# Kernel optimization log

Measured on AMD Instinct MI355X. Metric: run time of the kernel, lower is better.

## Reference

```python
import jax, jax.numpy as jnp
import numpy as np

N_NODES = 100000
N_EDGES = 3200000
EMB_DIM = 128


def setup_inputs() -> dict:
    key = jax.random.key(0)
    k_emb, k_w1, k_w2, k_e = jax.random.split(key, 4)
    emb = jax.random.normal(k_emb, (N_NODES, EMB_DIM), dtype=jnp.float32)
    W1 = jax.random.normal(k_w1, (EMB_DIM, 64), dtype=jnp.float32) * (1.0 / np.sqrt(EMB_DIM))
    b1 = jnp.zeros((64,), dtype=jnp.float32)
    W2 = jax.random.normal(k_w2, (64, 32), dtype=jnp.float32) * (1.0 / np.sqrt(64))
    b2 = jnp.zeros((32,), dtype=jnp.float32)
    edge_index = jax.random.randint(k_e, (2, N_EDGES), 0, N_NODES, dtype=jnp.int64)
    return {"embedding": emb, "W1": W1, "b1": b1, "W2": W2, "b2": b2,
            "edge_index": edge_index}


def gcn_conv(x, W, b, src, dst, n):
    # PyG GCNConv defaults: add self-loops, symmetric normalization D^-1/2 (A+I) D^-1/2,
    # linear transform first, then gather-scale-scatter aggregation, then bias.
    xw = x @ W                                                  # [N, out]
    ones = jnp.ones(src.shape, dtype=xw.dtype)
    deg = jax.ops.segment_sum(ones, dst, num_segments=n) + 1.0  # in-degree + self-loop
    dis = jax.lax.rsqrt(deg)                                    # deg >= 1 always
    norm = dis[src] * dis[dst]                                  # [E]
    agg = jax.ops.segment_sum(xw[src] * norm[:, None], dst, num_segments=n)
    agg = agg + (dis * dis)[:, None] * xw                       # self-loop messages
    return agg + b


def reference(embedding, W1, b1, W2, b2, edge_index):
    n = embedding.shape[0]
    src, dst = edge_index[0], edge_index[1]
    # encode
    h = jax.nn.relu(gcn_conv(embedding, W1, b1, src, dst, n))
    z = gcn_conv(h, W2, b2, src, dst, n)                        # [N, 32]
    # decode: per-edge gather-dot-sigmoid
    logits = jnp.sum(z[src] * z[dst], axis=1)                   # [E]
    return jax.nn.sigmoid(logits)
```

## Files before the change

kernel.cpp:

```cpp
#include <hip/hip_runtime.h>
#include <hip/hip_bf16.h>
#include <math.h>

#define NN 100000
#define NE 3200000
#define NPAD 100096
#define NB 196
#define BN 512
#define EPB 8192
#define NBLK 391

typedef __attribute__((ext_vector_type(8))) short short8;
typedef __attribute__((ext_vector_type(4))) float floatx4;

__device__ __forceinline__ unsigned short bf16_of(float x) {
    __hip_bfloat16 h = __float2bfloat16(x);
    return *(unsigned short*)&h;
}
__device__ __forceinline__ unsigned pack2(float a, float b) {
    return (unsigned)bf16_of(a) | ((unsigned)bf16_of(b) << 16);
}
__device__ __forceinline__ float lo_f(unsigned u) { return __uint_as_float(u << 16); }
__device__ __forceinline__ float hi_f(unsigned u) { return __uint_as_float(u & 0xffff0000u); }
__device__ __forceinline__ void acc8(float* a, uint4 r) {
    a[0] += lo_f(r.x); a[1] += hi_f(r.x);
    a[2] += lo_f(r.y); a[3] += hi_f(r.y);
    a[4] += lo_f(r.z); a[5] += hi_f(r.z);
    a[6] += lo_f(r.w); a[7] += hi_f(r.w);
}

__global__ __launch_bounds__(256) void hist_kernel(const int* __restrict__ dst,
                                                   int* __restrict__ blkhist) {
    __shared__ int cnt[NB];
    int t = threadIdx.x;
    for (int i = t; i < NB; i += 256) cnt[i] = 0;
    __syncthreads();
    int e0 = blockIdx.x * EPB;
    int e1 = min(e0 + EPB, NE);
    for (int e = e0 + t; e < e1; e += 256) atomicAdd(&cnt[dst[e] >> 9], 1);
    __syncthreads();
    for (int i = t; i < NB; i += 256) blkhist[i * NBLK + blockIdx.x] = cnt[i];
}

__global__ __launch_bounds__(64) void scanA_kernel(int* __restrict__ blkhist,
                                                   int* __restrict__ totals) {
    int j = blockIdx.x, lane = threadIdx.x;
    int base = j * NBLK;
    int carry = 0;
    for (int c = 0; c < NBLK; c += 64) {
        int b = c + lane;
        int v = (b < NBLK) ? blkhist[base + b] : 0;
        int inc = v;
#pragma unroll
        for (int m = 1; m < 64; m <<= 1) {
            int u = __shfl_up(inc, m, 64);
            if (lane >= m) inc += u;
        }
        if (b < NBLK) blkhist[base + b] = carry + inc - v;
        carry += __shfl(inc, 63, 64);
    }
    if (lane == 0) totals[j] = carry;
}

__global__ __launch_bounds__(256) void scanB_kernel(const int* __restrict__ totals,
                                                    int* __restrict__ bucket_base) {
    __shared__ int sm[NB];
    int t = threadIdx.x;
    if (t < NB) sm[t] = totals[t];
    __syncthreads();
    if (t == 0) {
        int r = 0;
        for (int i = 0; i < NB; ++i) { bucket_base[i] = r; r += sm[i]; }
        bucket_base[NB] = r;
    }
}

__global__ __launch_bounds__(256) void scatter_kernel(const int* __restrict__ src,
                                                      const int* __restrict__ dst,
                                                      const int* __restrict__ blkhist,
                                                      const int* __restrict__ bucket_base,
                                                      int* __restrict__ staged) {
    __shared__ int cnt[NB];
    __shared__ int lbase[NB + 1];
    __shared__ int gbase[NB];
    __shared__ int sbuf[EPB];
    __shared__ unsigned char sbkt[EPB];
    int t = threadIdx.x;
    for (int i = t; i < NB; i += 256) cnt[i] = 0;
    __syncthreads();
    int e0 = blockIdx.x * EPB;
    int e1 = min(e0 + EPB, NE);
    int cn = e1 - e0;
    for (int e = e0 + t; e < e1; e += 256) atomicAdd(&cnt[dst[e] >> 9], 1);
    __syncthreads();
    if (t < 64) {
        int v[4]; int s = 0;
#pragma unroll
        for (int k = 0; k < 4; ++k) { int idx = t * 4 + k; v[k] = (idx < NB) ? cnt[idx] : 0; s += v[k]; }
        int inc = s;
#pragma unroll
        for (int m = 1; m < 64; m <<= 1) {
            int u = __shfl_up(inc, m, 64);
            if (t >= m) inc += u;
        }
        int run = inc - s;
#pragma unroll
        for (int k = 0; k < 4; ++k) { int idx = t * 4 + k; if (idx < NB) lbase[idx] = run; run += v[k]; }
        if (t == 63) lbase[NB] = inc;
    }
    __syncthreads();
    for (int i = t; i < NB; i += 256) {
        gbase[i] = bucket_base[i] + blkhist[i * NBLK + blockIdx.x];
        cnt[i] = lbase[i];
    }
    __syncthreads();
    for (int e = e0 + t; e < e1; e += 256) {
        int s = src[e], d = dst[e];
        int bk = d >> 9;
        int r = atomicAdd(&cnt[bk], 1);
        sbuf[r] = (s << 9) | (d & (BN - 1));
        sbkt[r] = (unsigned char)bk;
    }
    __syncthreads();
    for (int i = t; i < cn; i += 256) {
        int bk = sbkt[i];
        staged[gbase[bk] + i - lbase[bk]] = sbuf[i];
    }
}

__global__ __launch_bounds__(256) void fine_kernel(const int* __restrict__ staged,
                                                   const int* __restrict__ bucket_base,
                                                   int* __restrict__ offset,
                                                   float* __restrict__ dis,
                                                   int* __restrict__ csr_src) {
    __shared__ int hist[BN];
    __shared__ int offs[BN];
    __shared__ int cur[BN];
    int t = threadIdx.x, j = blockIdx.x;
    int bb = bucket_base[j], be = bucket_base[j + 1];
    for (int i = t; i < BN; i += 256) hist[i] = 0;
    __syncthreads();
    for (int e = bb + t; e < be; e += 256) atomicAdd(&hist[staged[e] & (BN - 1)], 1);
    __syncthreads();
    if (t < 64) {
        int v[8]; int s = 0;
#pragma unroll
        for (int k = 0; k < 8; ++k) { v[k] = hist[t * 8 + k]; s += v[k]; }
        int inc = s;
#pragma unroll
        for (int m = 1; m < 64; m <<= 1) {
            int u = __shfl_up(inc, m, 64);
            if (t >= m) inc += u;
        }
        int run = inc - s;
#pragma unroll
        for (int k = 0; k < 8; ++k) { offs[t * 8 + k] = run; run += v[k]; }
    }
    __syncthreads();
    for (int l = t; l < BN; l += 256) {
        cur[l] = offs[l];
        int n = j * BN + l;
        if (n < NN) {
            offset[n] = bb + offs[l];
            dis[n] = rsqrtf((float)hist[l] + 1.0f);
        }
    }
    if (j == NB - 1 && t == 0) offset[NN] = NE;
    __syncthreads();
    for (int e = bb + t; e < be; e += 256) {
        int p = staged[e];
        int r = atomicAdd(&cur[p & (BN - 1)], 1);
        csr_src[bb + r] = p >> 9;
    }
}

__global__ __launch_bounds__(256) void mm1_kernel(const float* __restrict__ x,
                                                  const float* __restrict__ W,
                                                  const float* __restrict__ dis,
                                                  unsigned short* __restrict__ y) {
    __shared__ unsigned short Wt[64][136];
    int t = threadIdx.x;
    for (int i = t; i < 128 * 64; i += 256) {
        int k = i >> 6, n = i & 63;
        Wt[n][k] = bf16_of(W[i]);
    }
    __syncthreads();
    int wave = t >> 6, lane = t & 63;
    int quad = lane >> 4, n16 = lane & 15;
    short8 bfr[4][4];
#pragma unroll
    for (int s = 0; s < 4; ++s)
#pragma unroll
        for (int tt = 0; tt < 4; ++tt)
            bfr[s][tt] = *(const short8*)&Wt[tt * 16 + n16][s * 32 + quad * 8];
    int tile0 = (blockIdx.x * 4 + wave) * 4;
#pragma unroll 1
    for (int it = 0; it < 4; ++it) {
        int tile = tile0 + it;
        if (tile >= 6250) break;
        int m0 = tile * 16;
        const float* xp = x + (size_t)(m0 + n16) * 128 + quad * 8;
        floatx4 acc0 = {0,0,0,0}, acc1 = {0,0,0,0}, acc2 = {0,0,0,0}, acc3 = {0,0,0,0};
#pragma unroll
        for (int s = 0; s < 4; ++s) {
            float4 lo = *(const float4*)(xp + s * 32);
            float4 hi = *(const float4*)(xp + s * 32 + 4);
            short8 a;
            a[0] = (short)bf16_of(lo.x); a[1] = (short)bf16_of(lo.y);
            a[2] = (short)bf16_of(lo.z); a[3] = (short)bf16_of(lo.w);
            a[4] = (short)bf16_of(hi.x); a[5] = (short)bf16_of(hi.y);
            a[6] = (short)bf16_of(hi.z); a[7] = (short)bf16_of(hi.w);
            acc0 = __builtin_amdgcn_mfma_f32_16x16x32_bf16(a, bfr[s][0], acc0, 0, 0, 0);
            acc1 = __builtin_amdgcn_mfma_f32_16x16x32_bf16(a, bfr[s][1], acc1, 0, 0, 0);
            acc2 = __builtin_amdgcn_mfma_f32_16x16x32_bf16(a, bfr[s][2], acc2, 0, 0, 0);
            acc3 = __builtin_amdgcn_mfma_f32_16x16x32_bf16(a, bfr[s][3], acc3, 0, 0, 0);
        }
#pragma unroll
        for (int r = 0; r < 4; ++r) {
            int ro = m0 + quad * 4 + r;
            float sc = dis[ro];
            unsigned short* yp = y + (size_t)ro * 64 + n16;
            yp[0]  = bf16_of(acc0[r] * sc);
            yp[16] = bf16_of(acc1[r] * sc);
            yp[32] = bf16_of(acc2[r] * sc);
            yp[48] = bf16_of(acc3[r] * sc);
        }
    }
}

__global__ __launch_bounds__(256) void mm2_kernel(const unsigned short* __restrict__ h,
                                                  const float* __restrict__ W,
                                                  const float* __restrict__ dis,
                                                  unsigned short* __restrict__ y) {
    __shared__ unsigned short Wt[32][72];
    int t = threadIdx.x;
    for (int i = t; i < 64 * 32; i += 256) {
        int k = i >> 5, n = i & 31;
        Wt[n][k] = bf16_of(W[i]);
    }
    __syncthreads();
    int wave = t >> 6, lane = t & 63;
    int quad = lane >> 4, n16 = lane & 15;
    short8 bfr[2][2];
#pragma unroll
    for (int s = 0; s < 2; ++s)
#pragma unroll
        for (int tt = 0; tt < 2; ++tt)
            bfr[s][tt] = *(const short8*)&Wt[tt * 16 + n16][s * 32 + quad * 8];
    int tile0 = (blockIdx.x * 4 + wave) * 4;
#pragma unroll 1
    for (int it = 0; it < 4; ++it) {
        int tile = tile0 + it;
        if (tile >= 6250) break;
        int m0 = tile * 16;
        const unsigned short* hp = h + (size_t)(m0 + n16) * 64 + quad * 8;
        floatx4 acc0 = {0,0,0,0}, acc1 = {0,0,0,0};
#pragma unroll
        for (int s = 0; s < 2; ++s) {
            short8 a = *(const short8*)(hp + s * 32);
            acc0 = __builtin_amdgcn_mfma_f32_16x16x32_bf16(a, bfr[s][0], acc0, 0, 0, 0);
            acc1 = __builtin_amdgcn_mfma_f32_16x16x32_bf16(a, bfr[s][1], acc1, 0, 0, 0);
        }
#pragma unroll
        for (int r = 0; r < 4; ++r) {
            int ro = m0 + quad * 4 + r;
            float sc = dis[ro];
            unsigned short* yp = y + (size_t)ro * 32 + n16;
            yp[0]  = bf16_of(acc0[r] * sc);
            yp[16] = bf16_of(acc1[r] * sc);
        }
    }
}

__global__ __launch_bounds__(256) void agg64_kernel(const uint4* __restrict__ ys4,
                                                    const float* __restrict__ dis,
                                                    const int* __restrict__ offset,
                                                    const int* __restrict__ csr_src,
                                                    const float* __restrict__ b,
                                                    uint4* __restrict__ h4) {
    int tid = blockIdx.x * 256 + threadIdx.x;
    int nd = tid >> 3, c = tid & 7;
    if (nd >= NN) return;
    int start = offset[nd], end = offset[nd + 1];
    float acc[8] = {0, 0, 0, 0, 0, 0, 0, 0};
    acc8(acc, ys4[(size_t)nd * 8 + c]);
    int i = start;
    int n8 = start + ((end - start) & ~7);
    for (; i < n8; i += 8) {
        int s0 = csr_src[i],     s1 = csr_src[i + 1], s2 = csr_src[i + 2], s3 = csr_src[i + 3];
        int s4 = csr_src[i + 4], s5 = csr_src[i + 5], s6 = csr_src[i + 6], s7 = csr_src[i + 7];
        uint4 r0 = ys4[(size_t)s0 * 8 + c];
        uint4 r1 = ys4[(size_t)s1 * 8 + c];
        uint4 r2 = ys4[(size_t)s2 * 8 + c];
        uint4 r3 = ys4[(size_t)s3 * 8 + c];
        uint4 r4 = ys4[(size_t)s4 * 8 + c];
        uint4 r5 = ys4[(size_t)s5 * 8 + c];
        uint4 r6 = ys4[(size_t)s6 * 8 + c];
        uint4 r7 = ys4[(size_t)s7 * 8 + c];
        acc8(acc, r0); acc8(acc, r1); acc8(acc, r2); acc8(acc, r3);
        acc8(acc, r4); acc8(acc, r5); acc8(acc, r6); acc8(acc, r7);
    }
    for (; i < end; ++i) acc8(acc, ys4[(size_t)csr_src[i] * 8 + c]);
    float ds = dis[nd];
    const float4 bv0 = *(const float4*)&b[c * 8];
    const float4 bv1 = *(const float4*)&b[c * 8 + 4];
    uint4 o;
    o.x = pack2(fmaxf(fmaf(ds, acc[0], bv0.x), 0.f), fmaxf(fmaf(ds, acc[1], bv0.y), 0.f));
    o.y = pack2(fmaxf(fmaf(ds, acc[2], bv0.z), 0.f), fmaxf(fmaf(ds, acc[3], bv0.w), 0.f));
    o.z = pack2(fmaxf(fmaf(ds, acc[4], bv1.x), 0.f), fmaxf(fmaf(ds, acc[5], bv1.y), 0.f));
    o.w = pack2(fmaxf(fmaf(ds, acc[6], bv1.z), 0.f), fmaxf(fmaf(ds, acc[7], bv1.w), 0.f));
    h4[(size_t)nd * 8 + c] = o;
}

__global__ __launch_bounds__(256) void agg32_kernel(const uint4* __restrict__ ys4,
                                                    const float* __restrict__ dis,
                                                    const int* __restrict__ offset,
                                                    const int* __restrict__ csr_src,
                                                    const float* __restrict__ b,
                                                    uint4* __restrict__ z4) {
    int tid = blockIdx.x * 256 + threadIdx.x;
    int nd = tid >> 2, c = tid & 3;
    if (nd >= NN) return;
    int start = offset[nd], end = offset[nd + 1];
    float acc[8] = {0, 0, 0, 0, 0, 0, 0, 0};
    acc8(acc, ys4[(size_t)nd * 4 + c]);
    int i = start;
    int n8 = start + ((end - start) & ~7);
    for (; i < n8; i += 8) {
        int s0 = csr_src[i],     s1 = csr_src[i + 1], s2 = csr_src[i + 2], s3 = csr_src[i + 3];
        int s4 = csr_src[i + 4], s5 = csr_src[i + 5], s6 = csr_src[i + 6], s7 = csr_src[i + 7];
        uint4 r0 = ys4[(size_t)s0 * 4 + c];
        uint4 r1 = ys4[(size_t)s1 * 4 + c];
        uint4 r2 = ys4[(size_t)s2 * 4 + c];
        uint4 r3 = ys4[(size_t)s3 * 4 + c];
        uint4 r4 = ys4[(size_t)s4 * 4 + c];
        uint4 r5 = ys4[(size_t)s5 * 4 + c];
        uint4 r6 = ys4[(size_t)s6 * 4 + c];
        uint4 r7 = ys4[(size_t)s7 * 4 + c];
        acc8(acc, r0); acc8(acc, r1); acc8(acc, r2); acc8(acc, r3);
        acc8(acc, r4); acc8(acc, r5); acc8(acc, r6); acc8(acc, r7);
    }
    for (; i < end; ++i) acc8(acc, ys4[(size_t)csr_src[i] * 4 + c]);
    float ds = dis[nd];
    const float4 bv0 = *(const float4*)&b[c * 8];
    const float4 bv1 = *(const float4*)&b[c * 8 + 4];
    uint4 o;
    o.x = pack2(fmaf(ds, acc[0], bv0.x), fmaf(ds, acc[1], bv0.y));
    o.y = pack2(fmaf(ds, acc[2], bv0.z), fmaf(ds, acc[3], bv0.w));
    o.z = pack2(fmaf(ds, acc[4], bv1.x), fmaf(ds, acc[5], bv1.y));
    o.w = pack2(fmaf(ds, acc[6], bv1.z), fmaf(ds, acc[7], bv1.w));
    z4[(size_t)nd * 4 + c] = o;
}

__global__ __launch_bounds__(256) void decode_kernel(const uint4* __restrict__ z4,
                                                     const int* __restrict__ src,
                                                     const int* __restrict__ dst,
                                                     float* __restrict__ out) {
    int tid = blockIdx.x * 256 + threadIdx.x;
    int e = tid >> 2, k = tid & 3;
    if (e >= NE) return;
    int s = src[e], d = dst[e];
    uint4 ra = z4[(size_t)s * 4 + k];
    uint4 rb = z4[(size_t)d * 4 + k];
    float acc;
    acc  = lo_f(ra.x) * lo_f(rb.x) + hi_f(ra.x) * hi_f(rb.x);
    acc += lo_f(ra.y) * lo_f(rb.y) + hi_f(ra.y) * hi_f(rb.y);
    acc += lo_f(ra.z) * lo_f(rb.z) + hi_f(ra.z) * hi_f(rb.z);
    acc += lo_f(ra.w) * lo_f(rb.w) + hi_f(ra.w) * hi_f(rb.w);
#pragma unroll
    for (int m = 2; m >= 1; m >>= 1) acc += __shfl_xor(acc, m, 4);
    if (k == 0) out[e] = 1.0f / (1.0f + expf(-acc));
}

extern "C" void kernel_launch(void* const* d_in, const int* in_sizes, int n_in,
                              void* d_out, int out_size, void* d_ws, size_t ws_size,
                              hipStream_t stream) {
    const float* emb = (const float*)d_in[0];
    const float* W1  = (const float*)d_in[1];
    const float* b1  = (const float*)d_in[2];
    const float* W2  = (const float*)d_in[3];
    const float* b2  = (const float*)d_in[4];
    const int*   ei  = (const int*)d_in[5];
    const int* src = ei;
    const int* dst = ei + NE;
    float* out = (float*)d_out;

    char* w = (char*)d_ws;
    int*   offset      = (int*)w;           w += (size_t)NPAD * 4;
    float* dis         = (float*)w;         w += (size_t)NPAD * 4;
    int*   bucket_base = (int*)w;           w += 1024;
    int*   totals      = (int*)w;           w += 1024;
    int*   blkhist     = (int*)w;           w += 307200;
    int*   csr_src     = (int*)w;           w += (size_t)NE * 4;
    int*   staged      = (int*)w;           w += (size_t)NE * 4;
    unsigned short* ysbuf = (unsigned short*)w; w += (size_t)NN * 64 * 2;
    unsigned short* h  = (unsigned short*)w;
    unsigned short* ys1 = ysbuf;
    unsigned short* ys2 = ysbuf;
    unsigned short* z   = ysbuf + (size_t)NN * 32;

    hist_kernel<<<NBLK, 256, 0, stream>>>(dst, blkhist);
    scanA_kernel<<<NB, 64, 0, stream>>>(blkhist, totals);
    scanB_kernel<<<1, 256, 0, stream>>>(totals, bucket_base);
    scatter_kernel<<<NBLK, 256, 0, stream>>>(src, dst, blkhist, bucket_base, staged);
    fine_kernel<<<NB, 256, 0, stream>>>(staged, bucket_base, offset, dis, csr_src);

    mm1_kernel<<<391, 256, 0, stream>>>(emb, W1, dis, ys1);
    agg64_kernel<<<(NN * 8) / 256, 256, 0, stream>>>((const uint4*)ys1, dis, offset, csr_src, b1, (uint4*)h);

    mm2_kernel<<<391, 256, 0, stream>>>(h, W2, dis, ys2);
    agg32_kernel<<<(NN * 4 + 255) / 256, 256, 0, stream>>>((const uint4*)ys2, dis, offset, csr_src, b2, (uint4*)z);

    decode_kernel<<<(NE * 4) / 256, 256, 0, stream>>>((const uint4*)z, src, dst, out);
}
```

Measured before the change: 363.3 us.

## Split feature tables into 16-column chunks for cache-resident gathers; finer CSR buckets

Stores the transformed node features in a column-chunked layout (16 bf16 columns per chunk, one 3.2 MB slab per chunk) so each aggregation and decode pass gathers from a table small enough to stay in cache. Aggregation becomes one generic kernel launched per chunk, and decode runs in two passes that accumulate a partial dot product in a scratch buffer. The CSR build also moves to 256-node buckets and stages each bucket in LDS in the fine kernel to avoid re-reading it from global memory. The cost is more kernel launches, rereading the CSR indices and edge lists once per chunk, and an extra partial-sum round trip in decode.

```diff
diff --git a/kernel.cpp b/kernel.cpp
--- a/kernel.cpp
+++ b/kernel.cpp
@@ -5,10 +5,11 @@
 #define NN 100000
 #define NE 3200000
 #define NPAD 100096
-#define NB 196
-#define BN 512
+#define NB 391
+#define BN 256
 #define EPB 8192
 #define NBLK 391
+#define SBUF 9728
 
 typedef __attribute__((ext_vector_type(8))) short short8;
 typedef __attribute__((ext_vector_type(4))) float floatx4;
@@ -22,12 +23,6 @@
 }
 __device__ __forceinline__ float lo_f(unsigned u) { return __uint_as_float(u << 16); }
 __device__ __forceinline__ float hi_f(unsigned u) { return __uint_as_float(u & 0xffff0000u); }
-__device__ __forceinline__ void acc8(float* a, uint4 r) {
-    a[0] += lo_f(r.x); a[1] += hi_f(r.x);
-    a[2] += lo_f(r.y); a[3] += hi_f(r.y);
-    a[4] += lo_f(r.z); a[5] += hi_f(r.z);
-    a[6] += lo_f(r.w); a[7] += hi_f(r.w);
-}
 
 __global__ __launch_bounds__(256) void hist_kernel(const int* __restrict__ dst,
                                                    int* __restrict__ blkhist) {
@@ -37,7 +32,7 @@
     __syncthreads();
     int e0 = blockIdx.x * EPB;
     int e1 = min(e0 + EPB, NE);
-    for (int e = e0 + t; e < e1; e += 256) atomicAdd(&cnt[dst[e] >> 9], 1);
+    for (int e = e0 + t; e < e1; e += 256) atomicAdd(&cnt[dst[e] >> 8], 1);
     __syncthreads();
     for (int i = t; i < NB; i += 256) blkhist[i * NBLK + blockIdx.x] = cnt[i];
 }
@@ -66,7 +61,7 @@
                                                     int* __restrict__ bucket_base) {
     __shared__ int sm[NB];
     int t = threadIdx.x;
-    if (t < NB) sm[t] = totals[t];
+    for (int i = t; i < NB; i += 256) sm[i] = totals[i];
     __syncthreads();
     if (t == 0) {
         int r = 0;
@@ -84,19 +79,19 @@
     __shared__ int lbase[NB + 1];
     __shared__ int gbase[NB];
     __shared__ int sbuf[EPB];
-    __shared__ unsigned char sbkt[EPB];
+    __shared__ unsigned short sbkt[EPB];
     int t = threadIdx.x;
     for (int i = t; i < NB; i += 256) cnt[i] = 0;
     __syncthreads();
     int e0 = blockIdx.x * EPB;
     int e1 = min(e0 + EPB, NE);
     int cn = e1 - e0;
-    for (int e = e0 + t; e < e1; e += 256) atomicAdd(&cnt[dst[e] >> 9], 1);
+    for (int e = e0 + t; e < e1; e += 256) atomicAdd(&cnt[dst[e] >> 8], 1);
     __syncthreads();
     if (t < 64) {
-        int v[4]; int s = 0;
-#pragma unroll
-        for (int k = 0; k < 4; ++k) { int idx = t * 4 + k; v[k] = (idx < NB) ? cnt[idx] : 0; s += v[k]; }
+        int v[7]; int s = 0;
+#pragma unroll
+        for (int k = 0; k < 7; ++k) { int idx = t * 7 + k; v[k] = (idx < NB) ? cnt[idx] : 0; s += v[k]; }
         int inc = s;
 #pragma unroll
         for (int m = 1; m < 64; m <<= 1) {
@@ -105,7 +100,7 @@
         }
         int run = inc - s;
 #pragma unroll
-        for (int k = 0; k < 4; ++k) { int idx = t * 4 + k; if (idx < NB) lbase[idx] = run; run += v[k]; }
+        for (int k = 0; k < 7; ++k) { int idx = t * 7 + k; if (idx < NB) lbase[idx] = run; run += v[k]; }
         if (t == 63) lbase[NB] = inc;
     }
     __syncthreads();
@@ -116,10 +111,10 @@
     __syncthreads();
     for (int e = e0 + t; e < e1; e += 256) {
         int s = src[e], d = dst[e];
-        int bk = d >> 9;
+        int bk = d >> 8;
         int r = atomicAdd(&cnt[bk], 1);
-        sbuf[r] = (s << 9) | (d & (BN - 1));
-        sbkt[r] = (unsigned char)bk;
+        sbuf[r] = (s << 8) | (d & (BN - 1));
+        sbkt[r] = (unsigned short)bk;
     }
     __syncthreads();
     for (int i = t; i < cn; i += 256) {
@@ -136,16 +131,27 @@
     __shared__ int hist[BN];
     __shared__ int offs[BN];
     __shared__ int cur[BN];
+    __shared__ int sb[SBUF];
     int t = threadIdx.x, j = blockIdx.x;
     int bb = bucket_base[j], be = bucket_base[j + 1];
+    int cn = be - bb;
+    bool lds_ok = (cn <= SBUF);
     for (int i = t; i < BN; i += 256) hist[i] = 0;
     __syncthreads();
-    for (int e = bb + t; e < be; e += 256) atomicAdd(&hist[staged[e] & (BN - 1)], 1);
+    if (lds_ok) {
+        for (int e = t; e < cn; e += 256) {
+            int p = staged[bb + e];
+            sb[e] = p;
+            atomicAdd(&hist[p & (BN - 1)], 1);
+        }
+    } else {
+        for (int e = t; e < cn; e += 256) atomicAdd(&hist[staged[bb + e] & (BN - 1)], 1);
+    }
     __syncthreads();
     if (t < 64) {
-        int v[8]; int s = 0;
-#pragma unroll
-        for (int k = 0; k < 8; ++k) { v[k] = hist[t * 8 + k]; s += v[k]; }
+        int v[4]; int s = 0;
+#pragma unroll
+        for (int k = 0; k < 4; ++k) { v[k] = hist[t * 4 + k]; s += v[k]; }
         int inc = s;
 #pragma unroll
         for (int m = 1; m < 64; m <<= 1) {
@@ -154,23 +160,23 @@
         }
         int run = inc - s;
 #pragma unroll
-        for (int k = 0; k < 8; ++k) { offs[t * 8 + k] = run; run += v[k]; }
-    }
-    __syncthreads();
-    for (int l = t; l < BN; l += 256) {
-        cur[l] = offs[l];
-        int n = j * BN + l;
+        for (int k = 0; k < 4; ++k) { offs[t * 4 + k] = run; run += v[k]; }
+    }
+    __syncthreads();
+    if (t < BN) {
+        cur[t] = offs[t];
+        int n = j * BN + t;
         if (n < NN) {
-            offset[n] = bb + offs[l];
-            dis[n] = rsqrtf((float)hist[l] + 1.0f);
+            offset[n] = bb + offs[t];
+            dis[n] = rsqrtf((float)hist[t] + 1.0f);
         }
     }
     if (j == NB - 1 && t == 0) offset[NN] = NE;
     __syncthreads();
-    for (int e = bb + t; e < be; e += 256) {
-        int p = staged[e];
+    for (int e = t; e < cn; e += 256) {
+        int p = lds_ok ? sb[e] : staged[bb + e];
         int r = atomicAdd(&cur[p & (BN - 1)], 1);
-        csr_src[bb + r] = p >> 9;
+        csr_src[bb + r] = p >> 8;
     }
 }
 
@@ -219,11 +225,10 @@
         for (int r = 0; r < 4; ++r) {
             int ro = m0 + quad * 4 + r;
             float sc = dis[ro];
-            unsigned short* yp = y + (size_t)ro * 64 + n16;
-            yp[0]  = bf16_of(acc0[r] * sc);
-            yp[16] = bf16_of(acc1[r] * sc);
-            yp[32] = bf16_of(acc2[r] * sc);
-            yp[48] = bf16_of(acc3[r] * sc);
+            y[((size_t)0 * NN + ro) * 16 + n16] = bf16_of(acc0[r] * sc);
+            y[((size_t)1 * NN + ro) * 16 + n16] = bf16_of(acc1[r] * sc);
+            y[((size_t)2 * NN + ro) * 16 + n16] = bf16_of(acc2[r] * sc);
+            y[((size_t)3 * NN + ro) * 16 + n16] = bf16_of(acc3[r] * sc);
         }
     }
 }
@@ -253,11 +258,12 @@
         int tile = tile0 + it;
         if (tile >= 6250) break;
         int m0 = tile * 16;
-        const unsigned short* hp = h + (size_t)(m0 + n16) * 64 + quad * 8;
         floatx4 acc0 = {0,0,0,0}, acc1 = {0,0,0,0};
 #pragma unroll
         for (int s = 0; s < 2; ++s) {
-            short8 a = *(const short8*)(hp + s * 32);
+            const unsigned short* hp =
+                h + ((size_t)(s * 2 + (quad >> 1)) * NN + (m0 + n16)) * 16 + (quad & 1) * 8;
+            short8 a = *(const short8*)hp;
             acc0 = __builtin_amdgcn_mfma_f32_16x16x32_bf16(a, bfr[s][0], acc0, 0, 0, 0);
             acc1 = __builtin_amdgcn_mfma_f32_16x16x32_bf16(a, bfr[s][1], acc1, 0, 0, 0);
         }
@@ -265,111 +271,70 @@
         for (int r = 0; r < 4; ++r) {
             int ro = m0 + quad * 4 + r;
             float sc = dis[ro];
-            unsigned short* yp = y + (size_t)ro * 32 + n16;
-            yp[0]  = bf16_of(acc0[r] * sc);
-            yp[16] = bf16_of(acc1[r] * sc);
-        }
-    }
-}
-
-__global__ __launch_bounds__(256) void agg64_kernel(const uint4* __restrict__ ys4,
-                                                    const float* __restrict__ dis,
-                                                    const int* __restrict__ offset,
-                                                    const int* __restrict__ csr_src,
-                                                    const float* __restrict__ b,
-                                                    uint4* __restrict__ h4) {
+            y[((size_t)0 * NN + ro) * 16 + n16] = bf16_of(acc0[r] * sc);
+            y[((size_t)1 * NN + ro) * 16 + n16] = bf16_of(acc1[r] * sc);
+        }
+    }
+}
+
+__global__ __launch_bounds__(256) void aggc_kernel(const unsigned* __restrict__ ysp,
+                                                   const float* __restrict__ dis,
+                                                   const int* __restrict__ offset,
+                                                   const int* __restrict__ csr_src,
+                                                   const float* __restrict__ b,
+                                                   unsigned* __restrict__ outp,
+                                                   int do_relu) {
     int tid = blockIdx.x * 256 + threadIdx.x;
-    int nd = tid >> 3, c = tid & 7;
+    int nd = tid >> 3, c8 = tid & 7;
     if (nd >= NN) return;
     int start = offset[nd], end = offset[nd + 1];
-    float acc[8] = {0, 0, 0, 0, 0, 0, 0, 0};
-    acc8(acc, ys4[(size_t)nd * 8 + c]);
+    float a0, a1;
+    { unsigned u = ysp[nd * 8 + c8]; a0 = lo_f(u); a1 = hi_f(u); }
     int i = start;
     int n8 = start + ((end - start) & ~7);
     for (; i < n8; i += 8) {
         int s0 = csr_src[i],     s1 = csr_src[i + 1], s2 = csr_src[i + 2], s3 = csr_src[i + 3];
         int s4 = csr_src[i + 4], s5 = csr_src[i + 5], s6 = csr_src[i + 6], s7 = csr_src[i + 7];
-        uint4 r0 = ys4[(size_t)s0 * 8 + c];
-        uint4 r1 = ys4[(size_t)s1 * 8 + c];
-        uint4 r2 = ys4[(size_t)s2 * 8 + c];
-        uint4 r3 = ys4[(size_t)s3 * 8 + c];
-        uint4 r4 = ys4[(size_t)s4 * 8 + c];
-        uint4 r5 = ys4[(size_t)s5 * 8 + c];
-        uint4 r6 = ys4[(size_t)s6 * 8 + c];
-        uint4 r7 = ys4[(size_t)s7 * 8 + c];
-        acc8(acc, r0); acc8(acc, r1); acc8(acc, r2); acc8(acc, r3);
-        acc8(acc, r4); acc8(acc, r5); acc8(acc, r6); acc8(acc, r7);
-    }
-    for (; i < end; ++i) acc8(acc, ys4[(size_t)csr_src[i] * 8 + c]);
+        unsigned u0 = ysp[s0 * 8 + c8], u1 = ysp[s1 * 8 + c8];
+        unsigned u2 = ysp[s2 * 8 + c8], u3 = ysp[s3 * 8 + c8];
+        unsigned u4 = ysp[s4 * 8 + c8], u5 = ysp[s5 * 8 + c8];
+        unsigned u6 = ysp[s6 * 8 + c8], u7 = ysp[s7 * 8 + c8];
+        a0 += lo_f(u0); a1 += hi_f(u0); a0 += lo_f(u1); a1 += hi_f(u1);
+        a0 += lo_f(u2); a1 += hi_f(u2); a0 += lo_f(u3); a1 += hi_f(u3);
+        a0 += lo_f(u4); a1 += hi_f(u4); a0 += lo_f(u5); a1 += hi_f(u5);
+        a0 += lo_f(u6); a1 += hi_f(u6); a0 += lo_f(u7); a1 += hi_f(u7);
+    }
+    for (; i < end; ++i) {
+        unsigned u = ysp[csr_src[i] * 8 + c8];
+        a0 += lo_f(u); a1 += hi_f(u);
+    }
     float ds = dis[nd];
-    const float4 bv0 = *(const float4*)&b[c * 8];
-    const float4 bv1 = *(const float4*)&b[c * 8 + 4];
-    uint4 o;
-    o.x = pack2(fmaxf(fmaf(ds, acc[0], bv0.x), 0.f), fmaxf(fmaf(ds, acc[1], bv0.y), 0.f));
-    o.y = pack2(fmaxf(fmaf(ds, acc[2], bv0.z), 0.f), fmaxf(fmaf(ds, acc[3], bv0.w), 0.f));
-    o.z = pack2(fmaxf(fmaf(ds, acc[4], bv1.x), 0.f), fmaxf(fmaf(ds, acc[5], bv1.y), 0.f));
-    o.w = pack2(fmaxf(fmaf(ds, acc[6], bv1.z), 0.f), fmaxf(fmaf(ds, acc[7], bv1.w), 0.f));
-    h4[(size_t)nd * 8 + c] = o;
-}
-
-__global__ __launch_bounds__(256) void agg32_kernel(const uint4* __restrict__ ys4,
-                                                    const float* __restrict__ dis,
-                                                    const int* __restrict__ offset,
-                                                    const int* __restrict__ csr_src,
-                                                    const float* __restrict__ b,
-                                                    uint4* __restrict__ z4) {
-    int tid = blockIdx.x * 256 + threadIdx.x;
-    int nd = tid >> 2, c = tid & 3;
-    if (nd >= NN) return;
-    int start = offset[nd], end = offset[nd + 1];
-    float acc[8] = {0, 0, 0, 0, 0, 0, 0, 0};
-    acc8(acc, ys4[(size_t)nd * 4 + c]);
-    int i = start;
-    int n8 = start + ((end - start) & ~7);
-    for (; i < n8; i += 8) {
-        int s0 = csr_src[i],     s1 = csr_src[i + 1], s2 = csr_src[i + 2], s3 = csr_src[i + 3];
-        int s4 = csr_src[i + 4], s5 = csr_src[i + 5], s6 = csr_src[i + 6], s7 = csr_src[i + 7];
-        uint4 r0 = ys4[(size_t)s0 * 4 + c];
-        uint4 r1 = ys4[(size_t)s1 * 4 + c];
-        uint4 r2 = ys4[(size_t)s2 * 4 + c];
-        uint4 r3 = ys4[(size_t)s3 * 4 + c];
-        uint4 r4 = ys4[(size_t)s4 * 4 + c];
-        uint4 r5 = ys4[(size_t)s5 * 4 + c];
-        uint4 r6 = ys4[(size_t)s6 * 4 + c];
-        uint4 r7 = ys4[(size_t)s7 * 4 + c];
-        acc8(acc, r0); acc8(acc, r1); acc8(acc, r2); acc8(acc, r3);
-        acc8(acc, r4); acc8(acc, r5); acc8(acc, r6); acc8(acc, r7);
-    }
-    for (; i < end; ++i) acc8(acc, ys4[(size_t)csr_src[i] * 4 + c]);
-    float ds = dis[nd];
-    const float4 bv0 = *(const float4*)&b[c * 8];
-    const float4 bv1 = *(const float4*)&b[c * 8 + 4];
-    uint4 o;
-    o.x = pack2(fmaf(ds, acc[0], bv0.x), fmaf(ds, acc[1], bv0.y));
-    o.y = pack2(fmaf(ds, acc[2], bv0.z), fmaf(ds, acc[3], bv0.w));
-    o.z = pack2(fmaf(ds, acc[4], bv1.x), fmaf(ds, acc[5], bv1.y));
-    o.w = pack2(fmaf(ds, acc[6], bv1.z), fmaf(ds, acc[7], bv1.w));
-    z4[(size_t)nd * 4 + c] = o;
-}
-
-__global__ __launch_bounds__(256) void decode_kernel(const uint4* __restrict__ z4,
-                                                     const int* __restrict__ src,
-                                                     const int* __restrict__ dst,
-                                                     float* __restrict__ out) {
+    float r0 = fmaf(ds, a0, b[c8 * 2]);
+    float r1 = fmaf(ds, a1, b[c8 * 2 + 1]);
+    if (do_relu) { r0 = fmaxf(r0, 0.f); r1 = fmaxf(r1, 0.f); }
+    outp[nd * 8 + c8] = pack2(r0, r1);
+}
+
+__global__ __launch_bounds__(256) void decodec_kernel(const uint2* __restrict__ zp,
+                                                      const int* __restrict__ src,
+                                                      const int* __restrict__ dst,
+                                                      float* __restrict__ partial,
+                                                      float* __restrict__ out,
+                                                      int final_) {
     int tid = blockIdx.x * 256 + threadIdx.x;
     int e = tid >> 2, k = tid & 3;
     if (e >= NE) return;
     int s = src[e], d = dst[e];
-    uint4 ra = z4[(size_t)s * 4 + k];
-    uint4 rb = z4[(size_t)d * 4 + k];
-    float acc;
-    acc  = lo_f(ra.x) * lo_f(rb.x) + hi_f(ra.x) * hi_f(rb.x);
-    acc += lo_f(ra.y) * lo_f(rb.y) + hi_f(ra.y) * hi_f(rb.y);
-    acc += lo_f(ra.z) * lo_f(rb.z) + hi_f(ra.z) * hi_f(rb.z);
-    acc += lo_f(ra.w) * lo_f(rb.w) + hi_f(ra.w) * hi_f(rb.w);
-#pragma unroll
-    for (int m = 2; m >= 1; m >>= 1) acc += __shfl_xor(acc, m, 4);
-    if (k == 0) out[e] = 1.0f / (1.0f + expf(-acc));
+    uint2 za = zp[s * 4 + k];
+    uint2 zb = zp[d * 4 + k];
+    float acc = lo_f(za.x) * lo_f(zb.x) + hi_f(za.x) * hi_f(zb.x)
+              + lo_f(za.y) * lo_f(zb.y) + hi_f(za.y) * hi_f(zb.y);
+    acc += __shfl_xor(acc, 1, 4);
+    acc += __shfl_xor(acc, 2, 4);
+    if (k == 0) {
+        if (!final_) partial[e] = acc;
+        else out[e] = 1.0f / (1.0f + expf(-(partial[e] + acc)));
+    }
 }
 
 extern "C" void kernel_launch(void* const* d_in, const int* in_sizes, int n_in,
@@ -388,9 +353,9 @@
     char* w = (char*)d_ws;
     int*   offset      = (int*)w;           w += (size_t)NPAD * 4;
     float* dis         = (float*)w;         w += (size_t)NPAD * 4;
-    int*   bucket_base = (int*)w;           w += 1024;
-    int*   totals      = (int*)w;           w += 1024;
-    int*   blkhist     = (int*)w;           w += 307200;
+    int*   bucket_base = (int*)w;           w += 2048;
+    int*   totals      = (int*)w;           w += 2048;
+    int*   blkhist     = (int*)w;           w += (size_t)NB * NBLK * 4 + 1024;
     int*   csr_src     = (int*)w;           w += (size_t)NE * 4;
     int*   staged      = (int*)w;           w += (size_t)NE * 4;
     unsigned short* ysbuf = (unsigned short*)w; w += (size_t)NN * 64 * 2;
@@ -398,6 +363,7 @@
     unsigned short* ys1 = ysbuf;
     unsigned short* ys2 = ysbuf;
     unsigned short* z   = ysbuf + (size_t)NN * 32;
+    float* partial = (float*)staged;
 
     hist_kernel<<<NBLK, 256, 0, stream>>>(dst, blkhist);
     scanA_kernel<<<NB, 64, 0, stream>>>(blkhist, totals);
@@ -406,10 +372,18 @@
     fine_kernel<<<NB, 256, 0, stream>>>(staged, bucket_base, offset, dis, csr_src);
 
     mm1_kernel<<<391, 256, 0, stream>>>(emb, W1, dis, ys1);
-    agg64_kernel<<<(NN * 8) / 256, 256, 0, stream>>>((const uint4*)ys1, dis, offset, csr_src, b1, (uint4*)h);
+    for (int c = 0; c < 4; ++c)
+        aggc_kernel<<<(NN * 8 + 255) / 256, 256, 0, stream>>>(
+            (const unsigned*)(ys1 + (size_t)c * NN * 16), dis, offset, csr_src,
+            b1 + c * 16, (unsigned*)(h + (size_t)c * NN * 16), 1);
 
     mm2_kernel<<<391, 256, 0, stream>>>(h, W2, dis, ys2);
-    agg32_kernel<<<(NN * 4 + 255) / 256, 256, 0, stream>>>((const uint4*)ys2, dis, offset, csr_src, b2, (uint4*)z);
-
-    decode_kernel<<<(NE * 4) / 256, 256, 0, stream>>>((const uint4*)z, src, dst, out);
-}
+    for (int c = 0; c < 2; ++c)
+        aggc_kernel<<<(NN * 8 + 255) / 256, 256, 0, stream>>>(
+            (const unsigned*)(ys2 + (size_t)c * NN * 16), dis, offset, csr_src,
+            b2 + c * 16, (unsigned*)(z + (size_t)c * NN * 16), 0);
+
+    for (int p = 0; p < 2; ++p)
+        decodec_kernel<<<(NE * 4) / 256, 256, 0, stream>>>(
+            (const uint2*)(z + (size_t)p * NN * 16), src, dst, partial, out, p);
+}
```

New measurement: 446.2 us. +22.8%, slower.

## Decode edges in CSR order per destination node with fp16 dot2

Applied to the files above, without the earlier changes.

The decode stage now walks the CSR built for aggregation. One wavefront per destination node loads that node's z row once and reuses it across all incoming edges, and results are written back through a stored original edge id. This removes the random gather of z[dst] per edge but adds scattered output stores plus an extra edge-id array that must be staged and written. z is now stored as fp16 instead of bf16 so the dot product can use the packed fdot2 instruction. The bucket sort is rebuilt with 256-node buckets and 4096-edge scatter blocks, and it carries 8-byte staged entries.

```diff
diff --git a/kernel.cpp b/kernel.cpp
--- a/kernel.cpp
+++ b/kernel.cpp
@@ -5,13 +5,14 @@
 #define NN 100000
 #define NE 3200000
 #define NPAD 100096
-#define NB 196
-#define BN 512
-#define EPB 8192
-#define NBLK 391
+#define NB 391
+#define BN 256
+#define EPB 4096
+#define SBLK 782
 
 typedef __attribute__((ext_vector_type(8))) short short8;
 typedef __attribute__((ext_vector_type(4))) float floatx4;
+typedef _Float16 h2_t __attribute__((ext_vector_type(2)));
 
 __device__ __forceinline__ unsigned short bf16_of(float x) {
     __hip_bfloat16 h = __float2bfloat16(x);
@@ -29,6 +30,21 @@
     a[6] += lo_f(r.w); a[7] += hi_f(r.w);
 }
 
+__device__ __forceinline__ unsigned packh2(float a, float b) {
+    unsigned short ua = __builtin_bit_cast(unsigned short, (_Float16)a);
+    unsigned short ub = __builtin_bit_cast(unsigned short, (_Float16)b);
+    return (unsigned)ua | ((unsigned)ub << 16);
+}
+__device__ __forceinline__ float dot2acc(unsigned a, unsigned b, float acc) {
+#if __has_builtin(__builtin_amdgcn_fdot2)
+    return __builtin_amdgcn_fdot2(__builtin_bit_cast(h2_t, a),
+                                  __builtin_bit_cast(h2_t, b), acc, false);
+#else
+    h2_t ha = __builtin_bit_cast(h2_t, a), hb = __builtin_bit_cast(h2_t, b);
+    return acc + (float)ha[0] * (float)hb[0] + (float)ha[1] * (float)hb[1];
+#endif
+}
+
 __global__ __launch_bounds__(256) void hist_kernel(const int* __restrict__ dst,
                                                    int* __restrict__ blkhist) {
     __shared__ int cnt[NB];
@@ -37,26 +53,26 @@
     __syncthreads();
     int e0 = blockIdx.x * EPB;
     int e1 = min(e0 + EPB, NE);
-    for (int e = e0 + t; e < e1; e += 256) atomicAdd(&cnt[dst[e] >> 9], 1);
-    __syncthreads();
-    for (int i = t; i < NB; i += 256) blkhist[i * NBLK + blockIdx.x] = cnt[i];
+    for (int e = e0 + t; e < e1; e += 256) atomicAdd(&cnt[dst[e] >> 8], 1);
+    __syncthreads();
+    for (int i = t; i < NB; i += 256) blkhist[i * SBLK + blockIdx.x] = cnt[i];
 }
 
 __global__ __launch_bounds__(64) void scanA_kernel(int* __restrict__ blkhist,
                                                    int* __restrict__ totals) {
     int j = blockIdx.x, lane = threadIdx.x;
-    int base = j * NBLK;
+    int base = j * SBLK;
     int carry = 0;
-    for (int c = 0; c < NBLK; c += 64) {
+    for (int c = 0; c < SBLK; c += 64) {
         int b = c + lane;
-        int v = (b < NBLK) ? blkhist[base + b] : 0;
+        int v = (b < SBLK) ? blkhist[base + b] : 0;
         int inc = v;
 #pragma unroll
         for (int m = 1; m < 64; m <<= 1) {
             int u = __shfl_up(inc, m, 64);
             if (lane >= m) inc += u;
         }
-        if (b < NBLK) blkhist[base + b] = carry + inc - v;
+        if (b < SBLK) blkhist[base + b] = carry + inc - v;
         carry += __shfl(inc, 63, 64);
     }
     if (lane == 0) totals[j] = carry;
@@ -66,7 +82,7 @@
                                                     int* __restrict__ bucket_base) {
     __shared__ int sm[NB];
     int t = threadIdx.x;
-    if (t < NB) sm[t] = totals[t];
+    for (int i = t; i < NB; i += 256) sm[i] = totals[i];
     __syncthreads();
     if (t == 0) {
         int r = 0;
@@ -79,24 +95,24 @@
                                                       const int* __restrict__ dst,
                                                       const int* __restrict__ blkhist,
                                                       const int* __restrict__ bucket_base,
-                                                      int* __restrict__ staged) {
+                                                      int2* __restrict__ staged) {
     __shared__ int cnt[NB];
     __shared__ int lbase[NB + 1];
     __shared__ int gbase[NB];
-    __shared__ int sbuf[EPB];
-    __shared__ unsigned char sbkt[EPB];
+    __shared__ int2 sbuf[EPB];
+    __shared__ unsigned short sbkt[EPB];
     int t = threadIdx.x;
     for (int i = t; i < NB; i += 256) cnt[i] = 0;
     __syncthreads();
     int e0 = blockIdx.x * EPB;
     int e1 = min(e0 + EPB, NE);
     int cn = e1 - e0;
-    for (int e = e0 + t; e < e1; e += 256) atomicAdd(&cnt[dst[e] >> 9], 1);
+    for (int e = e0 + t; e < e1; e += 256) atomicAdd(&cnt[dst[e] >> 8], 1);
     __syncthreads();
     if (t < 64) {
-        int v[4]; int s = 0;
-#pragma unroll
-        for (int k = 0; k < 4; ++k) { int idx = t * 4 + k; v[k] = (idx < NB) ? cnt[idx] : 0; s += v[k]; }
+        int v[7]; int s = 0;
+#pragma unroll
+        for (int k = 0; k < 7; ++k) { int idx = t * 7 + k; v[k] = (idx < NB) ? cnt[idx] : 0; s += v[k]; }
         int inc = s;
 #pragma unroll
         for (int m = 1; m < 64; m <<= 1) {
@@ -105,21 +121,21 @@
         }
         int run = inc - s;
 #pragma unroll
-        for (int k = 0; k < 4; ++k) { int idx = t * 4 + k; if (idx < NB) lbase[idx] = run; run += v[k]; }
+        for (int k = 0; k < 7; ++k) { int idx = t * 7 + k; if (idx < NB) lbase[idx] = run; run += v[k]; }
         if (t == 63) lbase[NB] = inc;
     }
     __syncthreads();
     for (int i = t; i < NB; i += 256) {
-        gbase[i] = bucket_base[i] + blkhist[i * NBLK + blockIdx.x];
+        gbase[i] = bucket_base[i] + blkhist[i * SBLK + blockIdx.x];
         cnt[i] = lbase[i];
     }
     __syncthreads();
     for (int e = e0 + t; e < e1; e += 256) {
         int s = src[e], d = dst[e];
-        int bk = d >> 9;
+        int bk = d >> 8;
         int r = atomicAdd(&cnt[bk], 1);
-        sbuf[r] = (s << 9) | (d & (BN - 1));
-        sbkt[r] = (unsigned char)bk;
+        sbuf[r] = make_int2((s << 8) | (d & (BN - 1)), e);
+        sbkt[r] = (unsigned short)bk;
     }
     __syncthreads();
     for (int i = t; i < cn; i += 256) {
@@ -128,24 +144,26 @@
     }
 }
 
-__global__ __launch_bounds__(256) void fine_kernel(const int* __restrict__ staged,
+__global__ __launch_bounds__(256) void fine_kernel(const int2* __restrict__ staged,
                                                    const int* __restrict__ bucket_base,
                                                    int* __restrict__ offset,
                                                    float* __restrict__ dis,
-                                                   int* __restrict__ csr_src) {
+                                                   int* __restrict__ csr_src,
+                                                   int* __restrict__ csr_eid) {
     __shared__ int hist[BN];
     __shared__ int offs[BN];
     __shared__ int cur[BN];
     int t = threadIdx.x, j = blockIdx.x;
     int bb = bucket_base[j], be = bucket_base[j + 1];
+    int cn = be - bb;
     for (int i = t; i < BN; i += 256) hist[i] = 0;
     __syncthreads();
-    for (int e = bb + t; e < be; e += 256) atomicAdd(&hist[staged[e] & (BN - 1)], 1);
+    for (int e = t; e < cn; e += 256) atomicAdd(&hist[staged[bb + e].x & (BN - 1)], 1);
     __syncthreads();
     if (t < 64) {
-        int v[8]; int s = 0;
-#pragma unroll
-        for (int k = 0; k < 8; ++k) { v[k] = hist[t * 8 + k]; s += v[k]; }
+        int v[4]; int s = 0;
+#pragma unroll
+        for (int k = 0; k < 4; ++k) { v[k] = hist[t * 4 + k]; s += v[k]; }
         int inc = s;
 #pragma unroll
         for (int m = 1; m < 64; m <<= 1) {
@@ -154,23 +172,24 @@
         }
         int run = inc - s;
 #pragma unroll
-        for (int k = 0; k < 8; ++k) { offs[t * 8 + k] = run; run += v[k]; }
-    }
-    __syncthreads();
-    for (int l = t; l < BN; l += 256) {
-        cur[l] = offs[l];
-        int n = j * BN + l;
+        for (int k = 0; k < 4; ++k) { offs[t * 4 + k] = run; run += v[k]; }
+    }
+    __syncthreads();
+    if (t < BN) {
+        cur[t] = offs[t];
+        int n = j * BN + t;
         if (n < NN) {
-            offset[n] = bb + offs[l];
-            dis[n] = rsqrtf((float)hist[l] + 1.0f);
+            offset[n] = bb + offs[t];
+            dis[n] = rsqrtf((float)hist[t] + 1.0f);
         }
     }
     if (j == NB - 1 && t == 0) offset[NN] = NE;
     __syncthreads();
-    for (int e = bb + t; e < be; e += 256) {
-        int p = staged[e];
-        int r = atomicAdd(&cur[p & (BN - 1)], 1);
-        csr_src[bb + r] = p >> 9;
+    for (int e = t; e < cn; e += 256) {
+        int2 p = staged[bb + e];
+        int r = atomicAdd(&cur[p.x & (BN - 1)], 1);
+        csr_src[bb + r] = p.x >> 8;
+        csr_eid[bb + r] = p.y;
     }
 }
 
@@ -345,31 +364,34 @@
     const float4 bv0 = *(const float4*)&b[c * 8];
     const float4 bv1 = *(const float4*)&b[c * 8 + 4];
     uint4 o;
-    o.x = pack2(fmaf(ds, acc[0], bv0.x), fmaf(ds, acc[1], bv0.y));
-    o.y = pack2(fmaf(ds, acc[2], bv0.z), fmaf(ds, acc[3], bv0.w));
-    o.z = pack2(fmaf(ds, acc[4], bv1.x), fmaf(ds, acc[5], bv1.y));
-    o.w = pack2(fmaf(ds, acc[6], bv1.z), fmaf(ds, acc[7], bv1.w));
+    o.x = packh2(fmaf(ds, acc[0], bv0.x), fmaf(ds, acc[1], bv0.y));
+    o.y = packh2(fmaf(ds, acc[2], bv0.z), fmaf(ds, acc[3], bv0.w));
+    o.z = packh2(fmaf(ds, acc[4], bv1.x), fmaf(ds, acc[5], bv1.y));
+    o.w = packh2(fmaf(ds, acc[6], bv1.z), fmaf(ds, acc[7], bv1.w));
     z4[(size_t)nd * 4 + c] = o;
 }
 
 __global__ __launch_bounds__(256) void decode_kernel(const uint4* __restrict__ z4,
-                                                     const int* __restrict__ src,
-                                                     const int* __restrict__ dst,
+                                                     const int* __restrict__ offset,
+                                                     const int* __restrict__ csr_src,
+                                                     const int* __restrict__ csr_eid,
                                                      float* __restrict__ out) {
-    int tid = blockIdx.x * 256 + threadIdx.x;
-    int e = tid >> 2, k = tid & 3;
-    if (e >= NE) return;
-    int s = src[e], d = dst[e];
-    uint4 ra = z4[(size_t)s * 4 + k];
-    uint4 rb = z4[(size_t)d * 4 + k];
-    float acc;
-    acc  = lo_f(ra.x) * lo_f(rb.x) + hi_f(ra.x) * hi_f(rb.x);
-    acc += lo_f(ra.y) * lo_f(rb.y) + hi_f(ra.y) * hi_f(rb.y);
-    acc += lo_f(ra.z) * lo_f(rb.z) + hi_f(ra.z) * hi_f(rb.z);
-    acc += lo_f(ra.w) * lo_f(rb.w) + hi_f(ra.w) * hi_f(rb.w);
-#pragma unroll
-    for (int m = 2; m >= 1; m >>= 1) acc += __shfl_xor(acc, m, 4);
-    if (k == 0) out[e] = 1.0f / (1.0f + expf(-acc));
+    int wv = (blockIdx.x * 256 + threadIdx.x) >> 6;
+    if (wv >= NN) return;
+    int lane = threadIdx.x & 63, g = lane >> 2, k = lane & 3;
+    uint4 zd = z4[(size_t)wv * 4 + k];
+    int start = offset[wv], end = offset[wv + 1];
+    for (int i = start + g; i < end; i += 16) {
+        int s = csr_src[i];
+        uint4 za = z4[(size_t)s * 4 + k];
+        float acc = dot2acc(za.x, zd.x, 0.f);
+        acc = dot2acc(za.y, zd.y, acc);
+        acc = dot2acc(za.z, zd.z, acc);
+        acc = dot2acc(za.w, zd.w, acc);
+        acc += __shfl_xor(acc, 1, 4);
+        acc += __shfl_xor(acc, 2, 4);
+        if (k == 0) out[csr_eid[i]] = 1.0f / (1.0f + expf(-acc));
+    }
 }
 
 extern "C" void kernel_launch(void* const* d_in, const int* in_sizes, int n_in,
@@ -388,22 +410,23 @@
     char* w = (char*)d_ws;
     int*   offset      = (int*)w;           w += (size_t)NPAD * 4;
     float* dis         = (float*)w;         w += (size_t)NPAD * 4;
-    int*   bucket_base = (int*)w;           w += 1024;
-    int*   totals      = (int*)w;           w += 1024;
-    int*   blkhist     = (int*)w;           w += 307200;
+    int*   bucket_base = (int*)w;           w += 2048;
+    int*   totals      = (int*)w;           w += 2048;
+    int*   blkhist     = (int*)w;           w += (size_t)NB * SBLK * 4 + 1024;
     int*   csr_src     = (int*)w;           w += (size_t)NE * 4;
-    int*   staged      = (int*)w;           w += (size_t)NE * 4;
+    int*   csr_eid     = (int*)w;           w += (size_t)NE * 4;
+    int2*  staged      = (int2*)w;          w += (size_t)NE * 8;
     unsigned short* ysbuf = (unsigned short*)w; w += (size_t)NN * 64 * 2;
     unsigned short* h  = (unsigned short*)w;
     unsigned short* ys1 = ysbuf;
     unsigned short* ys2 = ysbuf;
     unsigned short* z   = ysbuf + (size_t)NN * 32;
 
-    hist_kernel<<<NBLK, 256, 0, stream>>>(dst, blkhist);
+    hist_kernel<<<SBLK, 256, 0, stream>>>(dst, blkhist);
     scanA_kernel<<<NB, 64, 0, stream>>>(blkhist, totals);
     scanB_kernel<<<1, 256, 0, stream>>>(totals, bucket_base);
-    scatter_kernel<<<NBLK, 256, 0, stream>>>(src, dst, blkhist, bucket_base, staged);
-    fine_kernel<<<NB, 256, 0, stream>>>(staged, bucket_base, offset, dis, csr_src);
+    scatter_kernel<<<SBLK, 256, 0, stream>>>(src, dst, blkhist, bucket_base, staged);
+    fine_kernel<<<NB, 256, 0, stream>>>(staged, bucket_base, offset, dis, csr_src, csr_eid);
 
     mm1_kernel<<<391, 256, 0, stream>>>(emb, W1, dis, ys1);
     agg64_kernel<<<(NN * 8) / 256, 256, 0, stream>>>((const uint4*)ys1, dis, offset, csr_src, b1, (uint4*)h);
@@ -411,5 +434,5 @@
     mm2_kernel<<<391, 256, 0, stream>>>(h, W2, dis, ys2);
     agg32_kernel<<<(NN * 4 + 255) / 256, 256, 0, stream>>>((const uint4*)ys2, dis, offset, csr_src, b2, (uint4*)z);
 
-    decode_kernel<<<(NE * 4) / 256, 256, 0, stream>>>((const uint4*)z, src, dst, out);
-}
+    decode_kernel<<<(NN * 64 + 255) / 256, 256, 0, stream>>>((const uint4*)z, offset, csr_src, csr_eid, out);
+}
```

After: 471.1 us. 1.3x slower.
